# Optimization experiments

Measured on AMD Instinct MI355X. Metric: run time of the kernel, lower is better.

## Reference

```python
import jax, jax.numpy as jnp
import numpy as np
import math

S, W, H = 256, 128, 768   # sentence, word, hidden (hidden fixed to 768 by PositionalEncoding)
TOPK = 3                  # len(inputs) > 2 branch: fuse 3 nearest sentences


def positional_encoding(length, d_model):
    # Standard sinusoidal PE, identical to the torch buffer construction.
    pos = jnp.arange(length, dtype=jnp.float32)[:, None]                      # [L,1]
    div = jnp.exp(jnp.arange(0, d_model, 2, dtype=jnp.float32)
                  * (-math.log(10000.0) / d_model))                           # [H/2]
    pe = jnp.zeros((length, d_model), dtype=jnp.float32)
    pe = pe.at[:, 0::2].set(jnp.sin(pos * div))
    pe = pe.at[:, 1::2].set(jnp.cos(pos * div))
    return pe


def setup_inputs() -> dict:
    key = jax.random.key(0)
    inputs = jax.random.normal(key, (S, W, H), dtype=jnp.float32)
    return {"inputs": inputs}


def reference(inputs):
    s, w, h = inputs.shape
    # Pairwise L1 distance between the FIRST word vector of each sentence
    # (matmulCell only ever sees x[i,0,:] and k[0,j,:] == inputs[j,0,:]).
    x0 = inputs[:, 0, :]                                                      # [S,H]
    dist = jnp.sum(jnp.abs(x0[:, None, :] - x0[None, :, :]), axis=-1)         # [S,S]
    # torch.sort ascending -> 3 nearest sentences (self included, dist 0)
    idx = jnp.argsort(dist, axis=1)[:, :TOPK]                                 # [S,3] int
    fused = inputs[idx].reshape(s, TOPK * w, h)                               # [S,3W,H]
    # Positional encoding added to both q/v stream and k stream (same tensor;
    # dropout p=0.1 is identity in eval mode).
    x = fused + positional_encoding(TOPK * w, h)[None]                        # [S,3W,H]
    # Scaled dot-product self-attention per row.
    scores = jnp.einsum('slh,smh->slm', x, x) / jnp.sqrt(jnp.float32(h))      # [S,3W,3W]
    attn = jax.nn.softmax(scores, axis=-1)
    out = jnp.einsum('slm,smh->slh', attn, x)                                 # [S,3W,H]
    # D_Attention keeps only the first word-1 rows of each fused output.
    return out[:, :w - 1, :]                                                  # [S,W-1,H]
```

## Files before the change

kernel.cpp:

```cpp
#include <hip/hip_runtime.h>

#define NS 256
#define NW 128
#define NH 768
#define NL 384
#define WH (NW*NH)
#define OUTROWS 127

typedef __attribute__((ext_vector_type(8))) short short8;
typedef __attribute__((ext_vector_type(8))) unsigned short ushort8;
typedef __attribute__((ext_vector_type(4))) float f32x4;

#define XS_STRIDE 72
#define PS_STRIDE 392
#define SMEM_PS   (NL*XS_STRIDE*2)
#define SMEM_RED  (SMEM_PS + 128*PS_STRIDE*2)
#define SMEM_TOTAL (SMEM_RED + 4096)

__device__ __forceinline__ unsigned short bf16b(float f) {
  union { float f; unsigned u; } x; x.f = f;
  return (unsigned short)((x.u + 0x7fffu + ((x.u >> 16) & 1u)) >> 16);
}
__device__ __forceinline__ float b2f(unsigned short h) {
  union { unsigned u; float f; } x; x.u = ((unsigned)h) << 16;
  return x.f;
}

__global__ __launch_bounds__(1024) void k_top3(const float* __restrict__ inp,
                                               int* __restrict__ idxw) {
  const int i = blockIdx.x, t = threadIdx.x;
  __shared__ float xi[772];
  __shared__ float dist[NS];
  __shared__ unsigned long long wkeys[16];
  for (int h = t; h < NH; h += 1024) xi[h + h / 192] = inp[(size_t)i * WH + h];
  __syncthreads();
  const int c = t >> 2, seg = t & 3;
  const float* __restrict__ row = inp + (size_t)c * WH + seg * 192;
  const float* xis = xi + seg * 193;
  float s = 0.f;
  #pragma unroll 4
  for (int h = 0; h < 192; h += 4) {
    float4 v = *(const float4*)(row + h);
    s += fabsf(xis[h]     - v.x) + fabsf(xis[h + 1] - v.y)
       + fabsf(xis[h + 2] - v.z) + fabsf(xis[h + 3] - v.w);
  }
  s += __shfl_xor(s, 1, 64);
  s += __shfl_xor(s, 2, 64);
  if (seg == 0) dist[c] = s;
  __syncthreads();
  for (int k = 0; k < 3; ++k) {
    float d = (t < NS) ? dist[t] : 3.4e38f;
    unsigned long long key = ((unsigned long long)__float_as_uint(d) << 32) | (unsigned)t;
    #pragma unroll
    for (int dd = 1; dd < 64; dd <<= 1) {
      unsigned long long o = __shfl_xor(key, dd, 64);
      key = (o < key) ? o : key;
    }
    if ((t & 63) == 0) wkeys[t >> 6] = key;
    __syncthreads();
    if (t == 0) {
      unsigned long long best = wkeys[0];
      for (int w = 1; w < 16; ++w) if (wkeys[w] < best) best = wkeys[w];
      int bj = (int)(best & 0xffffffffu);
      idxw[i * 3 + k] = bj;
      dist[bj] = 3.4e38f;
    }
    __syncthreads();
  }
}

__global__ __launch_bounds__(256) void k_pe(unsigned short* __restrict__ peb) {
  int gid = blockIdx.x * 256 + threadIdx.x;
  if (gid >= NL * NH) return;
  int l = gid / NH, d = gid - l * NH;
  const float c = -0.011992630687355995f;
  float dv = __expf((float)(d & ~1) * c);
  float ang = (float)l * dv;
  float v = (d & 1) ? cosf(ang) : sinf(ang);
  peb[gid] = bf16b(v);
}

__global__ __launch_bounds__(256) void k_inpb(const float* __restrict__ inp,
                                              unsigned short* __restrict__ inpb) {
  size_t gid = (size_t)blockIdx.x * 256 + threadIdx.x;
  size_t base = gid * 8;
  float4 a = *(const float4*)(inp + base);
  float4 b = *(const float4*)(inp + base + 4);
  ushort8 o;
  o[0] = bf16b(a.x); o[1] = bf16b(a.y); o[2] = bf16b(a.z); o[3] = bf16b(a.w);
  o[4] = bf16b(b.x); o[5] = bf16b(b.y); o[6] = bf16b(b.z); o[7] = bf16b(b.w);
  *(ushort8*)(inpb + base) = o;
}

template<bool BF>
__device__ __forceinline__ void load8(const void* __restrict__ src, size_t off, float* v) {
  if constexpr (BF) {
    ushort8 u = *reinterpret_cast<const ushort8*>((const unsigned short*)src + off);
    #pragma unroll
    for (int j = 0; j < 8; ++j) v[j] = b2f(u[j]);
  } else {
    float4 a = *reinterpret_cast<const float4*>((const float*)src + off);
    float4 b = *reinterpret_cast<const float4*>((const float*)src + off + 4);
    v[0] = a.x; v[1] = a.y; v[2] = a.z; v[3] = a.w;
    v[4] = b.x; v[5] = b.y; v[6] = b.z; v[7] = b.w;
  }
}

template<bool BF>
__global__ __launch_bounds__(512)
void k_attn(const void* __restrict__ xsrc, const unsigned short* __restrict__ peb,
            const int* __restrict__ idxw, float* __restrict__ out) {
  extern __shared__ char smem[];
  unsigned short* Xs = (unsigned short*)smem;
  unsigned short* Ps = (unsigned short*)(smem + SMEM_PS);
  float* red1 = (float*)(smem + SMEM_RED);
  float* red2 = red1 + 512;

  const int s = blockIdx.x;
  const int tid = threadIdx.x;
  const int lane = tid & 63, wid = tid >> 6;
  const int lrow = lane & 15, lhi = lane >> 4;
  const int i0 = idxw[s * 3 + 0], i1 = idxw[s * 3 + 1], i2 = idxw[s * 3 + 2];

  const f32x4 fz = {0.f, 0.f, 0.f, 0.f};
  f32x4 acc[4][6];
  #pragma unroll
  for (int qs = 0; qs < 4; ++qs)
    #pragma unroll
    for (int kf = 0; kf < 6; ++kf) acc[qs][kf] = fz;

  const int qh = wid & 1, kq = wid >> 1;

  for (int hc = 0; hc < 12; ++hc) {
    const int h0 = hc * 64;
    #pragma unroll
    for (int it = 0; it < 6; ++it) {
      const int src = (it < 2) ? i0 : (it < 4 ? i1 : i2);
      const int rl = (tid >> 3) + (it & 1) * 64;
      const int r  = rl + (it >> 1) * 128;
      const int c8 = (tid & 7) * 8;
      float xv[8], pv[8];
      load8<BF>(xsrc, (size_t)src * WH + (size_t)rl * NH + h0 + c8, xv);
      load8<true>(peb, (size_t)r * NH + h0 + c8, pv);
      ushort8 o;
      #pragma unroll
      for (int j = 0; j < 8; ++j) o[j] = bf16b(xv[j] + pv[j]);
      *reinterpret_cast<ushort8*>(&Xs[r * XS_STRIDE + c8]) = o;
    }
    __syncthreads();
    #pragma unroll
    for (int ks = 0; ks < 64; ks += 32) {
      short8 a[4];
      #pragma unroll
      for (int qs = 0; qs < 4; ++qs)
        a[qs] = *reinterpret_cast<const short8*>(&Xs[(qh * 64 + qs * 16 + lrow) * XS_STRIDE + ks + lhi * 8]);
      #pragma unroll
      for (int kf = 0; kf < 6; ++kf) {
        short8 b = *reinterpret_cast<const short8*>(&Xs[(kq * 96 + kf * 16 + lrow) * XS_STRIDE + ks + lhi * 8]);
        #pragma unroll
        for (int qs = 0; qs < 4; ++qs)
          acc[qs][kf] = __builtin_amdgcn_mfma_f32_16x16x32_bf16(a[qs], b, acc[qs][kf], 0, 0, 0);
      }
    }
    __syncthreads();
  }

  const float scale = 0.03608439182435161f;
  float mx[4][4];
  #pragma unroll
  for (int qs = 0; qs < 4; ++qs)
    #pragma unroll
    for (int r = 0; r < 4; ++r) {
      float m = acc[qs][0][r];
      #pragma unroll
      for (int kf = 1; kf < 6; ++kf) m = fmaxf(m, acc[qs][kf][r]);
      #pragma unroll
      for (int d = 1; d < 16; d <<= 1) m = fmaxf(m, __shfl_xor(m, d, 64));
      mx[qs][r] = m;
    }
  if (lrow == 0) {
    #pragma unroll
    for (int qs = 0; qs < 4; ++qs)
      #pragma unroll
      for (int r = 0; r < 4; ++r)
        red1[(qh * 64 + qs * 16 + lhi * 4 + r) * 4 + kq] = mx[qs][r];
  }
  __syncthreads();
  float sm[4][4];
  #pragma unroll
  for (int qs = 0; qs < 4; ++qs)
    #pragma unroll
    for (int r = 0; r < 4; ++r) {
      const int row = qh * 64 + qs * 16 + lhi * 4 + r;
      mx[qs][r] = fmaxf(fmaxf(red1[row * 4 + 0], red1[row * 4 + 1]),
                        fmaxf(red1[row * 4 + 2], red1[row * 4 + 3]));
      sm[qs][r] = 0.f;
    }
  #pragma unroll
  for (int qs = 0; qs < 4; ++qs)
    #pragma unroll
    for (int kf = 0; kf < 6; ++kf)
      #pragma unroll
      for (int r = 0; r < 4; ++r) {
        float p = __expf((acc[qs][kf][r] - mx[qs][r]) * scale);
        acc[qs][kf][r] = p;
        sm[qs][r] += p;
      }
  #pragma unroll
  for (int qs = 0; qs < 4; ++qs)
    #pragma unroll
    for (int r = 0; r < 4; ++r) {
      #pragma unroll
      for (int d = 1; d < 16; d <<= 1) sm[qs][r] += __shfl_xor(sm[qs][r], d, 64);
    }
  if (lrow == 0) {
    #pragma unroll
    for (int qs = 0; qs < 4; ++qs)
      #pragma unroll
      for (int r = 0; r < 4; ++r)
        red2[(qh * 64 + qs * 16 + lhi * 4 + r) * 4 + kq] = sm[qs][r];
  }
  __syncthreads();
  #pragma unroll
  for (int qs = 0; qs < 4; ++qs)
    #pragma unroll
    for (int r = 0; r < 4; ++r) {
      const int row = qh * 64 + qs * 16 + lhi * 4 + r;
      float t = red2[row * 4 + 0] + red2[row * 4 + 1] + red2[row * 4 + 2] + red2[row * 4 + 3];
      sm[qs][r] = 1.0f / t;
    }
  #pragma unroll
  for (int qs = 0; qs < 4; ++qs)
    #pragma unroll
    for (int kf = 0; kf < 6; ++kf)
      #pragma unroll
      for (int r = 0; r < 4; ++r)
        Ps[(qh * 64 + qs * 16 + lhi * 4 + r) * PS_STRIDE + kq * 96 + kf * 16 + lrow] =
            bf16b(acc[qs][kf][r] * sm[qs][r]);
  __syncthreads();

  const int qb = wid & 3, hh = wid >> 2;
  short8 pa[2][12];
  #pragma unroll
  for (int qs = 0; qs < 2; ++qs)
    #pragma unroll
    for (int m0 = 0; m0 < 12; ++m0)
      pa[qs][m0] = *reinterpret_cast<const short8*>(&Ps[(qb * 32 + qs * 16 + lrow) * PS_STRIDE + m0 * 32 + lhi * 8]);

  unsigned short* VT = Xs;
  for (int t4 = 0; t4 < 12; ++t4) {
    const int h0 = t4 * 64;
    #pragma unroll
    for (int it = 0; it < 6; ++it) {
      const int src = (it < 2) ? i0 : (it < 4 ? i1 : i2);
      const int ml = (tid >> 3) + (it & 1) * 64;
      const int m  = ml + (it >> 1) * 128;
      const int c8 = (tid & 7) * 8;
      float xv[8], pv[8];
      load8<BF>(xsrc, (size_t)src * WH + (size_t)ml * NH + h0 + c8, xv);
      load8<true>(peb, (size_t)m * NH + h0 + c8, pv);
      #pragma unroll
      for (int j = 0; j < 8; ++j) {
        const int vr = c8 + j;
        VT[((vr * PS_STRIDE) + m) ^ (((vr >> 3) & 7) << 3)] = bf16b(xv[j] + pv[j]);
      }
    }
    __syncthreads();
    f32x4 o00 = fz, o01 = fz, o10 = fz, o11 = fz;
    #pragma unroll
    for (int m0 = 0; m0 < 12; ++m0) {
      const int vr0 = hh * 32 + lrow, vr1 = vr0 + 16;
      short8 b0 = *reinterpret_cast<const short8*>(
          &VT[((vr0 * PS_STRIDE) + m0 * 32 + lhi * 8) ^ (((vr0 >> 3) & 7) << 3)]);
      short8 b1 = *reinterpret_cast<const short8*>(
          &VT[((vr1 * PS_STRIDE) + m0 * 32 + lhi * 8) ^ (((vr1 >> 3) & 7) << 3)]);
      o00 = __builtin_amdgcn_mfma_f32_16x16x32_bf16(pa[0][m0], b0, o00, 0, 0, 0);
      o01 = __builtin_amdgcn_mfma_f32_16x16x32_bf16(pa[0][m0], b1, o01, 0, 0, 0);
      o10 = __builtin_amdgcn_mfma_f32_16x16x32_bf16(pa[1][m0], b0, o10, 0, 0, 0);
      o11 = __builtin_amdgcn_mfma_f32_16x16x32_bf16(pa[1][m0], b1, o11, 0, 0, 0);
    }
    #pragma unroll
    for (int qs = 0; qs < 2; ++qs)
      #pragma unroll
      for (int hf = 0; hf < 2; ++hf) {
        f32x4 o = (qs == 0) ? (hf == 0 ? o00 : o01) : (hf == 0 ? o10 : o11);
        #pragma unroll
        for (int r = 0; r < 4; ++r) {
          const int q = qb * 32 + qs * 16 + lhi * 4 + r;
          if (q < OUTROWS)
            out[(size_t)s * (OUTROWS * NH) + (size_t)q * NH + h0 + hh * 32 + hf * 16 + lrow] = o[r];
        }
      }
    __syncthreads();
  }
}

extern "C" void kernel_launch(void* const* d_in, const int* in_sizes, int n_in,
                              void* d_out, int out_size, void* d_ws, size_t ws_size,
                              hipStream_t stream) {
  (void)in_sizes; (void)n_in; (void)out_size;
  const float* inp = (const float*)d_in[0];
  float* out = (float*)d_out;
  char* ws = (char*)d_ws;

  unsigned short* peb = (unsigned short*)ws;
  int* idxw           = (int*)(ws + 589824);
  unsigned short* inpb= (unsigned short*)(ws + 592896);
  const bool primary = ws_size >= (size_t)50924544;

  hipLaunchKernelGGL(k_top3, dim3(256), dim3(1024), 0, stream, inp, idxw);
  hipLaunchKernelGGL(k_pe, dim3(1152), dim3(256), 0, stream, peb);

  if (primary) {
    hipLaunchKernelGGL(k_inpb, dim3(12288), dim3(256), 0, stream, inp, inpb);
    hipFuncSetAttribute((const void*)k_attn<true>,
                        hipFuncAttributeMaxDynamicSharedMemorySize, SMEM_TOTAL);
    hipLaunchKernelGGL(k_attn<true>, dim3(256), dim3(512), SMEM_TOTAL, stream,
                       (const void*)inpb, peb, idxw, out);
  } else {
    hipFuncSetAttribute((const void*)k_attn<false>,
                        hipFuncAttributeMaxDynamicSharedMemorySize, SMEM_TOTAL);
    hipLaunchKernelGGL(k_attn<false>, dim3(256), dim3(512), SMEM_TOTAL, stream,
                       (const void*)inp, peb, idxw, out);
  }
}
```

Before: 138.9 us.

## Drop bf16 pre-conversion pass and double attention block to 1024 threads

```diff
diff --git a/kernel.cpp b/kernel.cpp
--- a/kernel.cpp
+++ b/kernel.cpp
@@ -9,6 +9,7 @@
 
 typedef __attribute__((ext_vector_type(8))) short short8;
 typedef __attribute__((ext_vector_type(8))) unsigned short ushort8;
+typedef __attribute__((ext_vector_type(8))) __bf16 bf16x8;
 typedef __attribute__((ext_vector_type(4))) float f32x4;
 
 #define XS_STRIDE 72
@@ -80,74 +81,50 @@
   peb[gid] = bf16b(v);
 }
 
-__global__ __launch_bounds__(256) void k_inpb(const float* __restrict__ inp,
-                                              unsigned short* __restrict__ inpb) {
-  size_t gid = (size_t)blockIdx.x * 256 + threadIdx.x;
-  size_t base = gid * 8;
-  float4 a = *(const float4*)(inp + base);
-  float4 b = *(const float4*)(inp + base + 4);
-  ushort8 o;
-  o[0] = bf16b(a.x); o[1] = bf16b(a.y); o[2] = bf16b(a.z); o[3] = bf16b(a.w);
-  o[4] = bf16b(b.x); o[5] = bf16b(b.y); o[6] = bf16b(b.z); o[7] = bf16b(b.w);
-  *(ushort8*)(inpb + base) = o;
-}
-
-template<bool BF>
-__device__ __forceinline__ void load8(const void* __restrict__ src, size_t off, float* v) {
-  if constexpr (BF) {
-    ushort8 u = *reinterpret_cast<const ushort8*>((const unsigned short*)src + off);
-    #pragma unroll
-    for (int j = 0; j < 8; ++j) v[j] = b2f(u[j]);
-  } else {
-    float4 a = *reinterpret_cast<const float4*>((const float*)src + off);
-    float4 b = *reinterpret_cast<const float4*>((const float*)src + off + 4);
-    v[0] = a.x; v[1] = a.y; v[2] = a.z; v[3] = a.w;
-    v[4] = b.x; v[5] = b.y; v[6] = b.z; v[7] = b.w;
-  }
-}
-
-template<bool BF>
-__global__ __launch_bounds__(512)
-void k_attn(const void* __restrict__ xsrc, const unsigned short* __restrict__ peb,
+__global__ __launch_bounds__(1024)
+void k_attn(const float* __restrict__ inp, const unsigned short* __restrict__ peb,
             const int* __restrict__ idxw, float* __restrict__ out) {
   extern __shared__ char smem[];
   unsigned short* Xs = (unsigned short*)smem;
   unsigned short* Ps = (unsigned short*)(smem + SMEM_PS);
-  float* red1 = (float*)(smem + SMEM_RED);
-  float* red2 = red1 + 512;
+  float* red = (float*)(smem + SMEM_RED);
+  float* xch = (float*)(smem + SMEM_PS);
 
   const int s = blockIdx.x;
   const int tid = threadIdx.x;
   const int lane = tid & 63, wid = tid >> 6;
   const int lrow = lane & 15, lhi = lane >> 4;
-  const int i0 = idxw[s * 3 + 0], i1 = idxw[s * 3 + 1], i2 = idxw[s * 3 + 2];
+  int idx3[3];
+  idx3[0] = idxw[s * 3 + 0]; idx3[1] = idxw[s * 3 + 1]; idx3[2] = idxw[s * 3 + 2];
 
   const f32x4 fz = {0.f, 0.f, 0.f, 0.f};
-  f32x4 acc[4][6];
-  #pragma unroll
-  for (int qs = 0; qs < 4; ++qs)
-    #pragma unroll
-    for (int kf = 0; kf < 6; ++kf) acc[qs][kf] = fz;
+  f32x4 acc[4][3];
+  #pragma unroll
+  for (int qs = 0; qs < 4; ++qs)
+    #pragma unroll
+    for (int kf = 0; kf < 3; ++kf) acc[qs][kf] = fz;
 
   const int qh = wid & 1, kq = wid >> 1;
+  const int rl = tid >> 3, c8 = (tid & 7) * 8;
 
   for (int hc = 0; hc < 12; ++hc) {
     const int h0 = hc * 64;
     #pragma unroll
-    for (int it = 0; it < 6; ++it) {
-      const int src = (it < 2) ? i0 : (it < 4 ? i1 : i2);
-      const int rl = (tid >> 3) + (it & 1) * 64;
-      const int r  = rl + (it >> 1) * 128;
-      const int c8 = (tid & 7) * 8;
-      float xv[8], pv[8];
-      load8<BF>(xsrc, (size_t)src * WH + (size_t)rl * NH + h0 + c8, xv);
-      load8<true>(peb, (size_t)r * NH + h0 + c8, pv);
-      ushort8 o;
-      #pragma unroll
-      for (int j = 0; j < 8; ++j) o[j] = bf16b(xv[j] + pv[j]);
-      *reinterpret_cast<ushort8*>(&Xs[r * XS_STRIDE + c8]) = o;
-    }
-    __syncthreads();
+    for (int it = 0; it < 3; ++it) {
+      const int r = rl + it * 128;
+      const float* px = inp + (size_t)idx3[it] * WH + (size_t)rl * NH + h0 + c8;
+      float4 a = *(const float4*)px;
+      float4 b = *(const float4*)(px + 4);
+      ushort8 pv = *(const ushort8*)&peb[r * NH + h0 + c8];
+      bf16x8 o;
+      o[0] = (__bf16)(a.x + b2f(pv[0])); o[1] = (__bf16)(a.y + b2f(pv[1]));
+      o[2] = (__bf16)(a.z + b2f(pv[2])); o[3] = (__bf16)(a.w + b2f(pv[3]));
+      o[4] = (__bf16)(b.x + b2f(pv[4])); o[5] = (__bf16)(b.y + b2f(pv[5]));
+      o[6] = (__bf16)(b.z + b2f(pv[6])); o[7] = (__bf16)(b.w + b2f(pv[7]));
+      *reinterpret_cast<bf16x8*>(&Xs[r * XS_STRIDE + c8]) = o;
+    }
+    __syncthreads();
+    __builtin_amdgcn_s_setprio(1);
     #pragma unroll
     for (int ks = 0; ks < 64; ks += 32) {
       short8 a[4];
@@ -155,13 +132,14 @@
       for (int qs = 0; qs < 4; ++qs)
         a[qs] = *reinterpret_cast<const short8*>(&Xs[(qh * 64 + qs * 16 + lrow) * XS_STRIDE + ks + lhi * 8]);
       #pragma unroll
-      for (int kf = 0; kf < 6; ++kf) {
-        short8 b = *reinterpret_cast<const short8*>(&Xs[(kq * 96 + kf * 16 + lrow) * XS_STRIDE + ks + lhi * 8]);
+      for (int kf = 0; kf < 3; ++kf) {
+        short8 b = *reinterpret_cast<const short8*>(&Xs[(kq * 48 + kf * 16 + lrow) * XS_STRIDE + ks + lhi * 8]);
         #pragma unroll
         for (int qs = 0; qs < 4; ++qs)
           acc[qs][kf] = __builtin_amdgcn_mfma_f32_16x16x32_bf16(a[qs], b, acc[qs][kf], 0, 0, 0);
       }
     }
+    __builtin_amdgcn_s_setprio(0);
     __syncthreads();
   }
 
@@ -173,7 +151,7 @@
     for (int r = 0; r < 4; ++r) {
       float m = acc[qs][0][r];
       #pragma unroll
-      for (int kf = 1; kf < 6; ++kf) m = fmaxf(m, acc[qs][kf][r]);
+      for (int kf = 1; kf < 3; ++kf) m = fmaxf(m, acc[qs][kf][r]);
       #pragma unroll
       for (int d = 1; d < 16; d <<= 1) m = fmaxf(m, __shfl_xor(m, d, 64));
       mx[qs][r] = m;
@@ -183,7 +161,7 @@
     for (int qs = 0; qs < 4; ++qs)
       #pragma unroll
       for (int r = 0; r < 4; ++r)
-        red1[(qh * 64 + qs * 16 + lhi * 4 + r) * 4 + kq] = mx[qs][r];
+        red[(qh * 64 + qs * 16 + lhi * 4 + r) * 8 + kq] = mx[qs][r];
   }
   __syncthreads();
   float sm[4][4];
@@ -192,14 +170,16 @@
     #pragma unroll
     for (int r = 0; r < 4; ++r) {
       const int row = qh * 64 + qs * 16 + lhi * 4 + r;
-      mx[qs][r] = fmaxf(fmaxf(red1[row * 4 + 0], red1[row * 4 + 1]),
-                        fmaxf(red1[row * 4 + 2], red1[row * 4 + 3]));
+      float4 m0 = *(const float4*)&red[row * 8];
+      float4 m1 = *(const float4*)&red[row * 8 + 4];
+      mx[qs][r] = fmaxf(fmaxf(fmaxf(m0.x, m0.y), fmaxf(m0.z, m0.w)),
+                        fmaxf(fmaxf(m1.x, m1.y), fmaxf(m1.z, m1.w)));
       sm[qs][r] = 0.f;
     }
   #pragma unroll
   for (int qs = 0; qs < 4; ++qs)
     #pragma unroll
-    for (int kf = 0; kf < 6; ++kf)
+    for (int kf = 0; kf < 3; ++kf)
       #pragma unroll
       for (int r = 0; r < 4; ++r) {
         float p = __expf((acc[qs][kf][r] - mx[qs][r]) * scale);
@@ -213,12 +193,13 @@
       #pragma unroll
       for (int d = 1; d < 16; d <<= 1) sm[qs][r] += __shfl_xor(sm[qs][r], d, 64);
     }
+  __syncthreads();
   if (lrow == 0) {
     #pragma unroll
     for (int qs = 0; qs < 4; ++qs)
       #pragma unroll
       for (int r = 0; r < 4; ++r)
-        red2[(qh * 64 + qs * 16 + lhi * 4 + r) * 4 + kq] = sm[qs][r];
+        red[(qh * 64 + qs * 16 + lhi * 4 + r) * 8 + kq] = sm[qs][r];
   }
   __syncthreads();
   #pragma unroll
@@ -226,101 +207,133 @@
     #pragma unroll
     for (int r = 0; r < 4; ++r) {
       const int row = qh * 64 + qs * 16 + lhi * 4 + r;
-      float t = red2[row * 4 + 0] + red2[row * 4 + 1] + red2[row * 4 + 2] + red2[row * 4 + 3];
+      float4 s0 = *(const float4*)&red[row * 8];
+      float4 s1 = *(const float4*)&red[row * 8 + 4];
+      float t = (s0.x + s0.y) + (s0.z + s0.w) + (s1.x + s1.y) + (s1.z + s1.w);
       sm[qs][r] = 1.0f / t;
     }
   #pragma unroll
   for (int qs = 0; qs < 4; ++qs)
     #pragma unroll
-    for (int kf = 0; kf < 6; ++kf)
-      #pragma unroll
-      for (int r = 0; r < 4; ++r)
-        Ps[(qh * 64 + qs * 16 + lhi * 4 + r) * PS_STRIDE + kq * 96 + kf * 16 + lrow] =
-            bf16b(acc[qs][kf][r] * sm[qs][r]);
-  __syncthreads();
-
-  const int qb = wid & 3, hh = wid >> 2;
-  short8 pa[2][12];
+    for (int kf = 0; kf < 3; ++kf)
+      #pragma unroll
+      for (int r = 0; r < 4; ++r) {
+        __bf16 pb = (__bf16)(acc[qs][kf][r] * sm[qs][r]);
+        Ps[(qh * 64 + qs * 16 + lhi * 4 + r) * PS_STRIDE + kq * 48 + kf * 16 + lrow] =
+            __builtin_bit_cast(unsigned short, pb);
+      }
+  __syncthreads();
+
+  const int qb = wid & 3, hh = (wid >> 2) & 1, ms = wid >> 3;
+  short8 pa[2][6];
   #pragma unroll
   for (int qs = 0; qs < 2; ++qs)
     #pragma unroll
-    for (int m0 = 0; m0 < 12; ++m0)
-      pa[qs][m0] = *reinterpret_cast<const short8*>(&Ps[(qb * 32 + qs * 16 + lrow) * PS_STRIDE + m0 * 32 + lhi * 8]);
+    for (int mm = 0; mm < 6; ++mm)
+      pa[qs][mm] = *reinterpret_cast<const short8*>(
+          &Ps[(qb * 32 + qs * 16 + lrow) * PS_STRIDE + ms * 192 + mm * 32 + lhi * 8]);
 
   unsigned short* VT = Xs;
+  const int g = lane & 7 ? 0 : 0;
+  (void)g;
+  const int gg = (lane >> 3) & 7;
+  const int jj = lane & 7;
+  const int m0p_base = wid * 8;
   for (int t4 = 0; t4 < 12; ++t4) {
     const int h0 = t4 * 64;
     #pragma unroll
-    for (int it = 0; it < 6; ++it) {
-      const int src = (it < 2) ? i0 : (it < 4 ? i1 : i2);
-      const int ml = (tid >> 3) + (it & 1) * 64;
-      const int m  = ml + (it >> 1) * 128;
-      const int c8 = (tid & 7) * 8;
-      float xv[8], pv[8];
-      load8<BF>(xsrc, (size_t)src * WH + (size_t)ml * NH + h0 + c8, xv);
-      load8<true>(peb, (size_t)m * NH + h0 + c8, pv);
-      #pragma unroll
-      for (int j = 0; j < 8; ++j) {
-        const int vr = c8 + j;
-        VT[((vr * PS_STRIDE) + m) ^ (((vr >> 3) & 7) << 3)] = bf16b(xv[j] + pv[j]);
-      }
-    }
-    __syncthreads();
-    f32x4 o00 = fz, o01 = fz, o10 = fz, o11 = fz;
-    #pragma unroll
-    for (int m0 = 0; m0 < 12; ++m0) {
-      const int vr0 = hh * 32 + lrow, vr1 = vr0 + 16;
-      short8 b0 = *reinterpret_cast<const short8*>(
-          &VT[((vr0 * PS_STRIDE) + m0 * 32 + lhi * 8) ^ (((vr0 >> 3) & 7) << 3)]);
-      short8 b1 = *reinterpret_cast<const short8*>(
-          &VT[((vr1 * PS_STRIDE) + m0 * 32 + lhi * 8) ^ (((vr1 >> 3) & 7) << 3)]);
-      o00 = __builtin_amdgcn_mfma_f32_16x16x32_bf16(pa[0][m0], b0, o00, 0, 0, 0);
-      o01 = __builtin_amdgcn_mfma_f32_16x16x32_bf16(pa[0][m0], b1, o01, 0, 0, 0);
-      o10 = __builtin_amdgcn_mfma_f32_16x16x32_bf16(pa[1][m0], b0, o10, 0, 0, 0);
-      o11 = __builtin_amdgcn_mfma_f32_16x16x32_bf16(pa[1][m0], b1, o11, 0, 0, 0);
-    }
-    #pragma unroll
-    for (int qs = 0; qs < 2; ++qs)
-      #pragma unroll
-      for (int hf = 0; hf < 2; ++hf) {
-        f32x4 o = (qs == 0) ? (hf == 0 ? o00 : o01) : (hf == 0 ? o10 : o11);
+    for (int it = 0; it < 3; ++it) {
+      const float* px = inp + (size_t)idx3[it] * WH + (size_t)rl * NH + h0 + c8;
+      float4 a = *(const float4*)px;
+      float4 b = *(const float4*)(px + 4);
+      ushort8 pv = *(const ushort8*)&peb[(rl + it * 128) * NH + h0 + c8];
+      float v[8];
+      v[0] = a.x + b2f(pv[0]); v[1] = a.y + b2f(pv[1]);
+      v[2] = a.z + b2f(pv[2]); v[3] = a.w + b2f(pv[3]);
+      v[4] = b.x + b2f(pv[4]); v[5] = b.y + b2f(pv[5]);
+      v[6] = b.z + b2f(pv[6]); v[7] = b.w + b2f(pv[7]);
+      #pragma unroll
+      for (int st = 0; st < 3; ++st) {
+        const int k = 1 << st;
         #pragma unroll
-        for (int r = 0; r < 4; ++r) {
-          const int q = qb * 32 + qs * 16 + lhi * 4 + r;
-          if (q < OUTROWS)
-            out[(size_t)s * (OUTROWS * NH) + (size_t)q * NH + h0 + hh * 32 + hf * 16 + lrow] = o[r];
+        for (int p = 0; p < 4; ++p) {
+          const int e0 = ((p & ~(k - 1)) << 1) | (p & (k - 1));
+          const int e1 = e0 | k;
+          const bool up = (gg & k) != 0;
+          float xs = up ? v[e0] : v[e1];
+          float y = __shfl_xor(xs, k * 8, 64);
+          v[e0] = up ? y : v[e0];
+          v[e1] = up ? v[e1] : y;
         }
       }
-    __syncthreads();
+      const int c = jj * 8 + gg;
+      const int m0p = m0p_base + it * 128;
+      bf16x8 w;
+      #pragma unroll
+      for (int e = 0; e < 8; ++e) w[e] = (__bf16)v[e];
+      *reinterpret_cast<bf16x8*>((char*)VT + (((c * PS_STRIDE + m0p) * 2) ^ (jj << 4))) = w;
+    }
+    __syncthreads();
+    __builtin_amdgcn_s_setprio(1);
+    f32x4 o00 = fz, o01 = fz, o10 = fz, o11 = fz;
+    const int vr0 = hh * 32 + lrow, vr1 = vr0 + 16;
+    const int sw0 = ((vr0 >> 3) & 7) << 4, sw1 = ((vr1 >> 3) & 7) << 4;
+    #pragma unroll
+    for (int mm = 0; mm < 6; ++mm) {
+      const int moff = (ms * 192 + mm * 32 + lhi * 8) * 2;
+      short8 b0 = *reinterpret_cast<const short8*>((const char*)VT + ((vr0 * PS_STRIDE * 2 + moff) ^ sw0));
+      short8 b1 = *reinterpret_cast<const short8*>((const char*)VT + ((vr1 * PS_STRIDE * 2 + moff) ^ sw1));
+      o00 = __builtin_amdgcn_mfma_f32_16x16x32_bf16(pa[0][mm], b0, o00, 0, 0, 0);
+      o01 = __builtin_amdgcn_mfma_f32_16x16x32_bf16(pa[0][mm], b1, o01, 0, 0, 0);
+      o10 = __builtin_amdgcn_mfma_f32_16x16x32_bf16(pa[1][mm], b0, o10, 0, 0, 0);
+      o11 = __builtin_amdgcn_mfma_f32_16x16x32_bf16(pa[1][mm], b1, o11, 0, 0, 0);
+    }
+    __builtin_amdgcn_s_setprio(0);
+    const int tb = qb * 2 + hh;
+    if (ms == 1) {
+      *(f32x4*)&xch[((0 * 8 + tb) * 64 + lane) * 4] = o00;
+      *(f32x4*)&xch[((1 * 8 + tb) * 64 + lane) * 4] = o01;
+      *(f32x4*)&xch[((2 * 8 + tb) * 64 + lane) * 4] = o10;
+      *(f32x4*)&xch[((3 * 8 + tb) * 64 + lane) * 4] = o11;
+    }
+    __syncthreads();
+    if (ms == 0) {
+      o00 += *(const f32x4*)&xch[((0 * 8 + tb) * 64 + lane) * 4];
+      o01 += *(const f32x4*)&xch[((1 * 8 + tb) * 64 + lane) * 4];
+      o10 += *(const f32x4*)&xch[((2 * 8 + tb) * 64 + lane) * 4];
+      o11 += *(const f32x4*)&xch[((3 * 8 + tb) * 64 + lane) * 4];
+      float* ob = out + (size_t)s * (OUTROWS * NH) + h0 + hh * 32 + lrow;
+      #pragma unroll
+      for (int qs = 0; qs < 2; ++qs)
+        #pragma unroll
+        for (int hf = 0; hf < 2; ++hf) {
+          f32x4 o = (qs == 0) ? (hf == 0 ? o00 : o01) : (hf == 0 ? o10 : o11);
+          #pragma unroll
+          for (int r = 0; r < 4; ++r) {
+            const int q = qb * 32 + qs * 16 + lhi * 4 + r;
+            if (q < OUTROWS) ob[(size_t)q * NH + hf * 16] = o[r];
+          }
+        }
+    }
   }
 }
 
 extern "C" void kernel_launch(void* const* d_in, const int* in_sizes, int n_in,
                               void* d_out, int out_size, void* d_ws, size_t ws_size,
                               hipStream_t stream) {
-  (void)in_sizes; (void)n_in; (void)out_size;
+  (void)in_sizes; (void)n_in; (void)out_size; (void)ws_size;
   const float* inp = (const float*)d_in[0];
   float* out = (float*)d_out;
   char* ws = (char*)d_ws;
 
   unsigned short* peb = (unsigned short*)ws;
   int* idxw           = (int*)(ws + 589824);
-  unsigned short* inpb= (unsigned short*)(ws + 592896);
-  const bool primary = ws_size >= (size_t)50924544;
 
   hipLaunchKernelGGL(k_top3, dim3(256), dim3(1024), 0, stream, inp, idxw);
   hipLaunchKernelGGL(k_pe, dim3(1152), dim3(256), 0, stream, peb);
 
-  if (primary) {
-    hipLaunchKernelGGL(k_inpb, dim3(12288), dim3(256), 0, stream, inp, inpb);
-    hipFuncSetAttribute((const void*)k_attn<true>,
-                        hipFuncAttributeMaxDynamicSharedMemorySize, SMEM_TOTAL);
-    hipLaunchKernelGGL(k_attn<true>, dim3(256), dim3(512), SMEM_TOTAL, stream,
-                       (const void*)inpb, peb, idxw, out);
-  } else {
-    hipFuncSetAttribute((const void*)k_attn<false>,
-                        hipFuncAttributeMaxDynamicSharedMemorySize, SMEM_TOTAL);
-    hipLaunchKernelGGL(k_attn<false>, dim3(256), dim3(512), SMEM_TOTAL, stream,
-                       (const void*)inp, peb, idxw, out);
-  }
-}
+  hipFuncSetAttribute((const void*)k_attn,
+                      hipFuncAttributeMaxDynamicSharedMemorySize, SMEM_TOTAL);
+  hipLaunchKernelGGL(k_attn, dim3(256), dim3(1024), SMEM_TOTAL, stream,
+                     inp, peb, idxw, out);
+}
```

After: 185.8 us. +33.8%, slower.
